# Performance work log

Hardware: AMD Instinct MI355X
Metric: run time of the kernel (lower is better)

The kernel has to match this reference:

```python
import jax, jax.numpy as jnp
import numpy as np

NEG_INIT = -1.0e9


def setup_inputs() -> dict:
    key = jax.random.key(0)
    k1, k2, k3, k4, k5, k6, k7 = jax.random.split(key, 7)
    N, D, d_att, G = 262144, 512, 128, 512
    feats = jax.random.normal(k1, (N, D), dtype=jnp.float32)
    index = jnp.sort(jax.random.randint(k2, (N,), 0, G, dtype=jnp.int64))
    # torch Linear params: weight (out,in), bias (out,)
    Vw = jax.random.normal(k3, (d_att, D), dtype=jnp.float32) / np.sqrt(D)
    Vb = jax.random.normal(k4, (d_att,), dtype=jnp.float32) * 0.01
    Uw = jax.random.normal(k5, (d_att, D), dtype=jnp.float32) / np.sqrt(D)
    Ub = jax.random.normal(k6, (d_att,), dtype=jnp.float32) * 0.01
    ww = jax.random.normal(k7, (1, d_att), dtype=jnp.float32) / np.sqrt(d_att)
    return {"feats": feats, "index": index, "num_groups": G,
            "Vw": Vw, "Vb": Vb, "Uw": Uw, "Ub": Ub, "ww": ww}


def reference(feats, index, num_groups, Vw, Vb, Uw, Ub, ww):
    # gated attention MLP: A = tanh(V x) * sigmoid(U x); scores = w A
    A = jnp.tanh(feats @ Vw.T + Vb) * jax.nn.sigmoid(feats @ Uw.T + Ub)  # (N, d_att)
    scores = (A @ ww.T)[:, 0]  # (N,)
    # segment max with -1e9 init (matches scatter_reduce amax include_self)
    max_per_group = jax.ops.segment_max(scores, index, num_segments=num_groups)
    max_per_group = jnp.maximum(max_per_group, NEG_INIT)  # empty segments -> -1e9
    exp_scores = jnp.exp(scores - max_per_group[index])
    denom = jax.ops.segment_sum(exp_scores, index, num_segments=num_groups)
    weights = exp_scores / (denom[index] + 1e-8)
    # weighted scatter-sum pooling: (num_groups, D)
    out = jax.ops.segment_sum(feats * weights[:, None], index, num_segments=num_groups)
    return out
```

## Files before the change

kernel.cpp:

```cpp
#include <hip/hip_runtime.h>
#include <hip/hip_fp8.h>
#include <cstddef>

#define NEG_INIT -1.0e9f

typedef _Float16 f16x8 __attribute__((ext_vector_type(8)));
typedef _Float16 f16x4 __attribute__((ext_vector_type(4)));
typedef _Float16 f16x2 __attribute__((ext_vector_type(2)));
typedef float f32x4 __attribute__((ext_vector_type(4)));

constexpr int D   = 512;
constexpr int BM  = 32;
constexpr int BK  = 32;
constexpr int NKS = D / BK;
constexpr int LDH = 520;
constexpr int LDR = 516;
constexpr int PS  = 516;
constexpr float RSC  = 2048.f;
constexpr float RISC = 1.f / 2048.f;

#if __has_builtin(__builtin_amdgcn_cvt_pk_fp8_f32) && __has_builtin(__builtin_amdgcn_cvt_f32_fp8)
#define HW_FP8 1
#else
#define HW_FP8 0
#endif

__device__ __forceinline__ unsigned int pack_fp8x4(float r0, float r1,
                                                   float r2, float r3) {
#if HW_FP8
    int p = __builtin_amdgcn_cvt_pk_fp8_f32(r0, r1, 0, false);
    p     = __builtin_amdgcn_cvt_pk_fp8_f32(r2, r3, p, true);
    return (unsigned int)p;
#else
    __hip_fp8_e4m3 q0(r0), q1(r1), q2(r2), q3(r3);
    return (unsigned int)q0.__x | ((unsigned int)q1.__x << 8) |
           ((unsigned int)q2.__x << 16) | ((unsigned int)q3.__x << 24);
#endif
}

template <int SEL>
__device__ __forceinline__ float unpack_fp8(unsigned int word) {
#if HW_FP8
    return __builtin_amdgcn_cvt_f32_fp8((int)word, SEL);
#else
    __hip_fp8_e4m3 q;
    q.__x = (unsigned char)(word >> (8 * SEL));
    return (float)q;
#endif
}

__global__ __launch_bounds__(64) void k_wprep(const float* __restrict__ Vw,
                                              const float* __restrict__ Uw,
                                              _Float16* __restrict__ Wfrag) {
    const int bid  = blockIdx.x;
    const int lane = threadIdx.x;
    const int j    = bid & 3;
    const int ks   = (bid >> 2) & 15;
    const int wc   = bid >> 6;
    const int l15  = lane & 15;
    const int kgrp = lane >> 4;
    const float* src = (j < 2 ? Vw + (size_t)(wc * 32 + j * 16 + l15) * D
                              : Uw + (size_t)(wc * 32 + (j - 2) * 16 + l15) * D)
                       + ks * BK + kgrp * 8;
    f16x8 h;
    #pragma unroll
    for (int e = 0; e < 8; ++e) h[e] = (_Float16)src[e];
    *(f16x8*)(Wfrag + ((size_t)bid * 64 + lane) * 8) = h;
}

__global__ __launch_bounds__(256) void k_bounds(const int* __restrict__ index,
                                                int N, int G,
                                                int* __restrict__ start) {
    int g = blockIdx.x * blockDim.x + threadIdx.x;
    if (g > G) return;
    int lo = 0, hi = N;
    while (lo < hi) {
        int mid = (lo + hi) >> 1;
        if (index[mid] < g) lo = mid + 1; else hi = mid;
    }
    start[g] = lo;
}

__global__ __launch_bounds__(512, 6) void k_fused(
    const float* __restrict__ feats, const _Float16* __restrict__ Wfrag,
    const float* __restrict__ Vb, const float* __restrict__ Ub,
    const float* __restrict__ ww, const int* __restrict__ index,
    const int* __restrict__ start, float* __restrict__ P, int N)
{
    __shared__ __align__(16) _Float16 Xh[BM][LDH];
    __shared__ __align__(4)  unsigned char Xr8[BM * LDR];
    __shared__ float sred[8][BM];
    __shared__ float srow[BM];
    __shared__ float evals[BM];

    const int t    = threadIdx.x;
    const int lane = t & 63;
    const int wc   = t >> 6;
    const int l15  = lane & 15;
    const int kgrp = lane >> 4;
    const int blk  = blockIdx.x;
    const int rb   = blk * BM;

    {
        const int xrow = t >> 4;
        const int xcb  = t & 15;
        const float* xg = feats + (size_t)min(rb + xrow, N - 1) * D + xcb * 4;
        #pragma unroll
        for (int k = 0; k < 8; ++k) {
            f32x4 v = *(const f32x4*)(xg + k * 64);
            f16x4 h;
            float res[4];
            #pragma unroll
            for (int e = 0; e < 4; ++e) {
                h[e] = (_Float16)v[e];
                res[e] = (v[e] - (float)h[e]) * RSC;
            }
            unsigned int rp = pack_fp8x4(res[0], res[1], res[2], res[3]);
            *(f16x4*)&Xh[xrow][k * 64 + xcb * 4] = h;
            *(unsigned int*)&Xr8[xrow * LDR + k * 64 + xcb * 4] = rp;
        }
    }
    __syncthreads();

    const _Float16* wbV = Wfrag + (size_t)(wc >> 1) * 32768
                                + (size_t)(wc & 1) * 512 + (size_t)lane * 8;
    const _Float16* wbU = wbV + 1024;

    f32x4 accV[2], accU[2];
    #pragma unroll
    for (int i = 0; i < 2; ++i) {
        accV[i] = (f32x4){0.f, 0.f, 0.f, 0.f};
        accU[i] = (f32x4){0.f, 0.f, 0.f, 0.f};
    }

    #pragma unroll 4
    for (int ks = 0; ks < NKS; ++ks) {
        f16x8 bv = *(const f16x8*)(wbV + (size_t)ks * 2048);
        f16x8 bu = *(const f16x8*)(wbU + (size_t)ks * 2048);
        f16x8 ha[2];
        #pragma unroll
        for (int i = 0; i < 2; ++i)
            ha[i] = *(const f16x8*)&Xh[i * 16 + l15][ks * BK + kgrp * 8];
        #pragma unroll
        for (int i = 0; i < 2; ++i) {
            accV[i] = __builtin_amdgcn_mfma_f32_16x16x32_f16(ha[i], bv, accV[i], 0, 0, 0);
            accU[i] = __builtin_amdgcn_mfma_f32_16x16x32_f16(ha[i], bu, accU[i], 0, 0, 0);
        }
    }

    {
        const int c = wc * 16 + l15;
        const float vb = Vb[c], ub = Ub[c], w = ww[c];
        float part[2][4];
        #pragma unroll
        for (int i = 0; i < 2; ++i)
            #pragma unroll
            for (int r = 0; r < 4; ++r) {
                float v = accV[i][r] + vb;
                float u = accU[i][r] + ub;
                part[i][r] = w * tanhf(v) * (1.f / (1.f + expf(-u)));
            }
        #pragma unroll
        for (int off = 1; off < 16; off <<= 1)
            #pragma unroll
            for (int i = 0; i < 2; ++i)
                #pragma unroll
                for (int r = 0; r < 4; ++r)
                    part[i][r] += __shfl_xor(part[i][r], off);
        if (l15 == 0) {
            #pragma unroll
            for (int i = 0; i < 2; ++i)
                #pragma unroll
                for (int r = 0; r < 4; ++r)
                    sred[wc][i * 16 + kgrp * 4 + r] = part[i][r];
        }
    }
    __syncthreads();
    if (t < BM) {
        float s = sred[0][t];
        #pragma unroll
        for (int w8 = 1; w8 < 8; ++w8) s += sred[w8][t];
        srow[t] = s;
    }
    __syncthreads();

    const int gl = index[rb];
    const int gh = index[rb + BM - 1];
    for (int g = gl + wc; g <= gh; g += 8) {
        const int r0 = max(start[g], rb), r1 = min(start[g + 1], rb + BM);
        if (r1 <= r0) continue;
        const bool in = (lane >= r0 - rb) && (lane < r1 - rb);
        float m = in ? srow[lane] : NEG_INIT;
        #pragma unroll
        for (int off = 32; off; off >>= 1) m = fmaxf(m, __shfl_xor(m, off));
        float e = in ? expf(srow[lane] - m) : 0.f;
        if (in) evals[lane] = e;
        float s = e;
        #pragma unroll
        for (int off = 32; off; off >>= 1) s += __shfl_xor(s, off);
        if (lane == 0) {
            float* slot = P + (size_t)(blk + g) * PS;
            slot[0] = m; slot[1] = s;
        }
    }
    __syncthreads();

    if (t < 256) {
        const int c0 = t * 2;
        for (int g = gl; g <= gh; ++g) {
            const int r0 = max(start[g], rb), r1 = min(start[g + 1], rb + BM);
            if (r1 <= r0) continue;
            float a0 = 0.f, a1 = 0.f;
            for (int r = r0; r < r1; ++r) {
                const int rr = r - rb;
                const float e = evals[rr];
                f16x2 hp = *(const f16x2*)&Xh[rr][c0];
                unsigned int rv = *(const unsigned short*)&Xr8[rr * LDR + c0];
                float x0 = fmaf(unpack_fp8<0>(rv), RISC, (float)hp[0]);
                float x1 = fmaf(unpack_fp8<1>(rv), RISC, (float)hp[1]);
                a0 = fmaf(e, x0, a0);
                a1 = fmaf(e, x1, a1);
            }
            float2 o = {a0, a1};
            *(float2*)(P + (size_t)(blk + g) * PS + 4 + c0) = o;
        }
    }
}

__global__ __launch_bounds__(512) void k_merge(const float* __restrict__ P,
                                               const int* __restrict__ start,
                                               float* __restrict__ out)
{
    const int g = blockIdx.x, t = threadIdx.x;
    const int s0 = start[g], s1 = start[g + 1];
    if (s0 >= s1) { out[(size_t)g * D + t] = 0.f; return; }
    const int b0 = s0 >> 5, b1 = (s1 - 1) >> 5;
    float M = NEG_INIT;
    for (int b = b0; b <= b1; ++b)
        M = fmaxf(M, P[(size_t)(b + g) * PS]);
    float den = 0.f, acc = 0.f;
    for (int b = b0; b <= b1; ++b) {
        const float* slot = P + (size_t)(b + g) * PS;
        float w = expf(slot[0] - M);
        den += w * slot[1];
        acc += w * slot[4 + t];
    }
    out[(size_t)g * D + t] = acc / (den + 1e-8f);
}

extern "C" void kernel_launch(void* const* d_in, const int* in_sizes, int n_in,
                              void* d_out, int out_size, void* d_ws, size_t ws_size,
                              hipStream_t stream) {
    const float* feats = (const float*)d_in[0];
    const int*   index = (const int*)d_in[1];
    const float* Vw = (const float*)d_in[3];
    const float* Vb = (const float*)d_in[4];
    const float* Uw = (const float*)d_in[5];
    const float* Ub = (const float*)d_in[6];
    const float* ww = (const float*)d_in[7];
    float* out = (float*)d_out;

    const int N = in_sizes[1];
    const int G = out_size / D;
    const int nblk = (N + BM - 1) / BM;

    _Float16* Wfrag = (_Float16*)d_ws;
    int* start      = (int*)(Wfrag + (size_t)256 * 512);
    size_t off      = (size_t)256 * 512 * 2 + (G + 1) * 4;
    off             = (off + 15) & ~(size_t)15;
    float* P        = (float*)((char*)d_ws + off);

    hipLaunchKernelGGL(k_wprep, dim3(256), dim3(64), 0, stream, Vw, Uw, Wfrag);
    hipLaunchKernelGGL(k_bounds, dim3((G + 1 + 255) / 256), dim3(256), 0, stream,
                       index, N, G, start);
    hipLaunchKernelGGL(k_fused, dim3(nblk), dim3(512), 0, stream,
                       feats, Wfrag, Vb, Ub, ww, index, start, P, N);
    hipLaunchKernelGGL(k_merge, dim3(G), dim3(512), 0, stream, P, start, out);
}
```

Baseline: 234.7 us.

## Pipeline feature staging with MFMA loop and use fast tanh/sigmoid

Splits the load of the feature tile into four 128-column stages that are double-buffered in registers. Each stage is converted to fp16 plus an fp8 residual and written to LDS while MFMAs run on the previous stage, using barriers that wait only on lgkmcnt. The goal is to hide global-load latency behind the matrix math. The gate activations also switch from tanhf/expf to __expf plus hardware reciprocal, which loses a little accuracy. The clamp on the last row index is removed, so a partial final block would read past the end of the input.

```diff
diff --git a/kernel.cpp b/kernel.cpp
--- a/kernel.cpp
+++ b/kernel.cpp
@@ -13,11 +13,20 @@
 constexpr int BM  = 32;
 constexpr int BK  = 32;
 constexpr int NKS = D / BK;
-constexpr int LDH = 520;
-constexpr int LDR = 516;
+constexpr int SSK = 4;
+constexpr int NSS = NKS / SSK;
+constexpr int LDH  = 520;
+constexpr int LDRB = 520;
 constexpr int PS  = 516;
 constexpr float RSC  = 2048.f;
 constexpr float RISC = 1.f / 2048.f;
+
+#define BAR_LGKM()                                            \
+    do {                                                      \
+        asm volatile("s_waitcnt lgkmcnt(0)" ::: "memory");    \
+        __builtin_amdgcn_s_barrier();                         \
+        asm volatile("" ::: "memory");                        \
+    } while (0)
 
 #if __has_builtin(__builtin_amdgcn_cvt_pk_fp8_f32) && __has_builtin(__builtin_amdgcn_cvt_f32_fp8)
 #define HW_FP8 1
@@ -47,6 +56,14 @@
     q.__x = (unsigned char)(word >> (8 * SEL));
     return (float)q;
 #endif
+}
+
+__device__ __forceinline__ float fast_tanh(float v) {
+    float e2 = __expf(2.f * v);
+    return 1.f - 2.f * __builtin_amdgcn_rcpf(e2 + 1.f);
+}
+__device__ __forceinline__ float fast_sigmoid(float u) {
+    return __builtin_amdgcn_rcpf(1.f + __expf(-u));
 }
 
 __global__ __launch_bounds__(64) void k_wprep(const float* __restrict__ Vw,
@@ -88,7 +105,7 @@
     const int* __restrict__ start, float* __restrict__ P, int N)
 {
     __shared__ __align__(16) _Float16 Xh[BM][LDH];
-    __shared__ __align__(4)  unsigned char Xr8[BM * LDR];
+    __shared__ __align__(8)  unsigned char Xr8[BM * LDRB];
     __shared__ float sred[8][BM];
     __shared__ float srow[BM];
     __shared__ float evals[BM];
@@ -101,26 +118,36 @@
     const int blk  = blockIdx.x;
     const int rb   = blk * BM;
 
-    {
-        const int xrow = t >> 4;
-        const int xcb  = t & 15;
-        const float* xg = feats + (size_t)min(rb + xrow, N - 1) * D + xcb * 4;
-        #pragma unroll
-        for (int k = 0; k < 8; ++k) {
-            f32x4 v = *(const f32x4*)(xg + k * 64);
-            f16x4 h;
-            float res[4];
-            #pragma unroll
-            for (int e = 0; e < 4; ++e) {
-                h[e] = (_Float16)v[e];
-                res[e] = (v[e] - (float)h[e]) * RSC;
-            }
-            unsigned int rp = pack_fp8x4(res[0], res[1], res[2], res[3]);
-            *(f16x4*)&Xh[xrow][k * 64 + xcb * 4] = h;
-            *(unsigned int*)&Xr8[xrow * LDR + k * 64 + xcb * 4] = rp;
-        }
-    }
-    __syncthreads();
+    const int srw  = t >> 4;
+    const int scol = (t & 15) * 8;
+    const float* xg = feats + (size_t)(rb + srw) * D + scol;
+
+    float4 xa[2][2];
+    auto issueX = [&](int ss) {
+        const float* p = xg + ss * 128;
+        xa[ss & 1][0] = *(const float4*)p;
+        xa[ss & 1][1] = *(const float4*)(p + 4);
+    };
+    auto commitX = [&](int ss) {
+        const int c0 = ss * 128 + scol;
+        float v[8];
+        v[0] = xa[ss & 1][0].x; v[1] = xa[ss & 1][0].y;
+        v[2] = xa[ss & 1][0].z; v[3] = xa[ss & 1][0].w;
+        v[4] = xa[ss & 1][1].x; v[5] = xa[ss & 1][1].y;
+        v[6] = xa[ss & 1][1].z; v[7] = xa[ss & 1][1].w;
+        f16x8 h;
+        float res[8];
+        #pragma unroll
+        for (int e = 0; e < 8; ++e) {
+            h[e] = (_Float16)v[e];
+            res[e] = (v[e] - (float)h[e]) * RSC;
+        }
+        unsigned int rp0 = pack_fp8x4(res[0], res[1], res[2], res[3]);
+        unsigned int rp1 = pack_fp8x4(res[4], res[5], res[6], res[7]);
+        *(f16x8*)&Xh[srw][c0] = h;
+        uint2 rw = {rp0, rp1};
+        *(uint2*)&Xr8[srw * LDRB + c0] = rw;
+    };
 
     const _Float16* wbV = Wfrag + (size_t)(wc >> 1) * 32768
                                 + (size_t)(wc & 1) * 512 + (size_t)lane * 8;
@@ -133,18 +160,31 @@
         accU[i] = (f32x4){0.f, 0.f, 0.f, 0.f};
     }
 
-    #pragma unroll 4
-    for (int ks = 0; ks < NKS; ++ks) {
-        f16x8 bv = *(const f16x8*)(wbV + (size_t)ks * 2048);
-        f16x8 bu = *(const f16x8*)(wbU + (size_t)ks * 2048);
-        f16x8 ha[2];
-        #pragma unroll
-        for (int i = 0; i < 2; ++i)
-            ha[i] = *(const f16x8*)&Xh[i * 16 + l15][ks * BK + kgrp * 8];
-        #pragma unroll
-        for (int i = 0; i < 2; ++i) {
-            accV[i] = __builtin_amdgcn_mfma_f32_16x16x32_f16(ha[i], bv, accV[i], 0, 0, 0);
-            accU[i] = __builtin_amdgcn_mfma_f32_16x16x32_f16(ha[i], bu, accU[i], 0, 0, 0);
+    issueX(0); issueX(1);
+    commitX(0);
+    BAR_LGKM();
+
+    #pragma unroll
+    for (int ss = 0; ss < NSS; ++ss) {
+        if (ss + 2 < NSS) issueX(ss + 2);
+        #pragma unroll
+        for (int k2 = 0; k2 < SSK; ++k2) {
+            const int ks = ss * SSK + k2;
+            f16x8 bv = *(const f16x8*)(wbV + (size_t)ks * 2048);
+            f16x8 bu = *(const f16x8*)(wbU + (size_t)ks * 2048);
+            f16x8 ha[2];
+            #pragma unroll
+            for (int i = 0; i < 2; ++i)
+                ha[i] = *(const f16x8*)&Xh[i * 16 + l15][ks * BK + kgrp * 8];
+            #pragma unroll
+            for (int i = 0; i < 2; ++i) {
+                accV[i] = __builtin_amdgcn_mfma_f32_16x16x32_f16(ha[i], bv, accV[i], 0, 0, 0);
+                accU[i] = __builtin_amdgcn_mfma_f32_16x16x32_f16(ha[i], bu, accU[i], 0, 0, 0);
+            }
+        }
+        if (ss + 1 < NSS) {
+            commitX(ss + 1);
+            BAR_LGKM();
         }
     }
 
@@ -158,7 +198,7 @@
             for (int r = 0; r < 4; ++r) {
                 float v = accV[i][r] + vb;
                 float u = accU[i][r] + ub;
-                part[i][r] = w * tanhf(v) * (1.f / (1.f + expf(-u)));
+                part[i][r] = w * fast_tanh(v) * fast_sigmoid(u);
             }
         #pragma unroll
         for (int off = 1; off < 16; off <<= 1)
@@ -215,7 +255,7 @@
                 const int rr = r - rb;
                 const float e = evals[rr];
                 f16x2 hp = *(const f16x2*)&Xh[rr][c0];
-                unsigned int rv = *(const unsigned short*)&Xr8[rr * LDR + c0];
+                unsigned int rv = *(const unsigned short*)&Xr8[rr * LDRB + c0];
                 float x0 = fmaf(unpack_fp8<0>(rv), RISC, (float)hp[0]);
                 float x1 = fmaf(unpack_fp8<1>(rv), RISC, (float)hp[1]);
                 a0 = fmaf(e, x0, a0);
```

Result: faster. 206.6 us, median of 2 (-12.0%).
